# Optimization experiments

Measured on AMD Instinct MI355X. Metric: run time of the kernel, lower is better.

## Reference

```python
import jax, jax.numpy as jnp
import numpy as np
from itertools import permutations

NUM_SPEAKERS = 4
EPS = 1e-07


def setup_inputs() -> dict:
    key = jax.random.key(0)
    k1, k2 = jax.random.split(key)
    B, T, S = 128, 16384, NUM_SPEAKERS
    pred = jax.random.uniform(k1, (B, T, S), dtype=jnp.float32)
    target = jax.random.uniform(k2, (B, T, S), dtype=jnp.float32)
    mask = jnp.ones((B, T), dtype=jnp.float32)
    return {"pred": pred, "target": target, "mask": mask}


def reference(pred, target, mask):
    # pred, target: [B, T, S]; mask: [B, T]
    B, T, S = pred.shape
    p = jnp.clip(pred, EPS, 1.0 - EPS)
    logp = jnp.log(p)          # [B,T,S]
    log1mp = jnp.log1p(-p)     # [B,T,S]
    # Pairwise BCE: bce[b,t,i,j] = -(target[b,t,j]*log p[b,t,i] + (1-target[b,t,j])*log(1-p[b,t,i]))
    bce = -(target[:, :, None, :] * logp[:, :, :, None]
            + (1.0 - target[:, :, None, :]) * log1mp[:, :, :, None])  # [B,T,S,S]
    denom = jnp.sum(mask, axis=1)  # [B]
    # Masked mean over time, mean over prediction-speaker axis i -> cost matrix C[b,i,j]
    C = jnp.einsum('btij,bt->bij', bce, mask) / (S * denom)[:, None, None]  # [B,S,S]
    perms = jnp.asarray(list(permutations(range(S))), dtype=jnp.int32)  # [P,S]
    # perm_losses[b,p] = sum_i C[b, i, perms[p,i]] / S? no: mean over i already folded via /S above
    idx_i = jnp.arange(S)[None, :]            # [1,S]
    perm_losses = jnp.sum(C[:, idx_i, perms], axis=-1)  # [B,P]
    min_loss = jnp.min(perm_losses, axis=-1)  # [B]
    best_idx = jnp.argmin(perm_losses, axis=-1)  # [B] index into perms
    loss = jnp.mean(min_loss)
    best_perms = perms[best_idx]  # [B,S]
    return loss, best_perms
```

## Files before the change

kernel.cpp:

```cpp
#include <hip/hip_runtime.h>

#define TPB    256
#define CHUNKS 8
#define NACC   21
#define NPERM  24

__constant__ int c_perm[NPERM][4] = {
    {0,1,2,3},{0,1,3,2},{0,2,1,3},{0,2,3,1},{0,3,1,2},{0,3,2,1},
    {1,0,2,3},{1,0,3,2},{1,2,0,3},{1,2,3,0},{1,3,0,2},{1,3,2,0},
    {2,0,1,3},{2,0,3,1},{2,1,0,3},{2,1,3,0},{2,3,0,1},{2,3,1,0},
    {3,0,1,2},{3,0,2,1},{3,1,0,2},{3,1,2,0},{3,2,0,1},{3,2,1,0}
};

__global__ __launch_bounds__(TPB) void pit_partial(
    const float* __restrict__ pred, const float* __restrict__ target,
    const float* __restrict__ mask, float* __restrict__ partial, int T, int nblk)
{
    const int b      = blockIdx.x / CHUNKS;
    const int chunk  = blockIdx.x - b * CHUNKS;
    const int tPerBlock = (T + CHUNKS - 1) / CHUNKS;
    const int tid    = threadIdx.x;
    const int base   = chunk * tPerBlock;
    const int tEnd   = min(base + tPerBlock, T);

    const float4* p4  = (const float4*)pred   + (size_t)b * T;
    const float4* t4  = (const float4*)target + (size_t)b * T;
    const float* mrow = mask + (size_t)b * T;

    float D[4][4] = {{0.f,0.f,0.f,0.f},{0.f,0.f,0.f,0.f},
                     {0.f,0.f,0.f,0.f},{0.f,0.f,0.f,0.f}};
    float S1[4] = {0.f,0.f,0.f,0.f};
    float dn = 0.f;

    const float lo = 1e-7f;
    const float hi = 1.0f - 1e-7f;

    auto body = [&](int t) {
        float4 pv = p4[t];
        float4 tv = t4[t];
        float m   = mrow[t];
        float pp[4] = {pv.x, pv.y, pv.z, pv.w};
        float tt[4] = {tv.x, tv.y, tv.z, tv.w};
        float lp[4], lq[4];
        #pragma unroll
        for (int s = 0; s < 4; ++s) {
            float p = fminf(fmaxf(pp[s], lo), hi);
            lp[s] = __logf(p);
            lq[s] = __logf(1.0f - p);
        }
        dn += m;
        float mt[4];
        #pragma unroll
        for (int j = 0; j < 4; ++j) mt[j] = m * tt[j];
        #pragma unroll
        for (int i = 0; i < 4; ++i) {
            S1[i] = fmaf(m, lq[i], S1[i]);
            float d = lq[i] - lp[i];
            #pragma unroll
            for (int j = 0; j < 4; ++j) D[i][j] = fmaf(d, mt[j], D[i][j]);
        }
    };

    int t = base + tid;
    for (; t + 3 * TPB < tEnd; t += 4 * TPB) {
        body(t);
        body(t + TPB);
        body(t + 2 * TPB);
        body(t + 3 * TPB);
    }
    for (; t < tEnd; t += TPB) body(t);

    float acc[NACC];
    #pragma unroll
    for (int i = 0; i < 4; ++i)
        #pragma unroll
        for (int j = 0; j < 4; ++j) acc[i * 4 + j] = D[i][j];
    #pragma unroll
    for (int i = 0; i < 4; ++i) acc[16 + i] = S1[i];
    acc[20] = dn;

    #pragma unroll
    for (int k = 0; k < NACC; ++k) {
        float v = acc[k];
        #pragma unroll
        for (int off = 32; off > 0; off >>= 1)
            v += __shfl_xor(v, off, 64);
        acc[k] = v;
    }

    __shared__ float sred[TPB / 64][NACC];
    const int wave = tid >> 6;
    const int lane = tid & 63;
    if (lane == 0) {
        #pragma unroll
        for (int k = 0; k < NACC; ++k) sred[wave][k] = acc[k];
    }
    __syncthreads();
    if (tid < NACC) {
        float v = 0.f;
        #pragma unroll
        for (int w = 0; w < TPB / 64; ++w) v += sred[w][tid];
        partial[(size_t)tid * nblk + blockIdx.x] = v;
    }
}

__global__ __launch_bounds__(128) void pit_final(
    const float* __restrict__ partial, float* __restrict__ out, int B, int nblk)
{
    const int b = threadIdx.x;
    float minv = 0.f;

    if (b < B) {
        float A[NACC];
        #pragma unroll
        for (int k = 0; k < NACC; ++k) {
            const float4* src =
                (const float4*)(partial + (size_t)k * nblk + b * CHUNKS);
            float4 u = src[0];
            float4 v = src[1];
            A[k] = ((u.x + u.y) + (u.z + u.w)) + ((v.x + v.y) + (v.z + v.w));
        }
        const float inv = 1.0f / (4.0f * A[20]);
        float C[4][4];
        #pragma unroll
        for (int i = 0; i < 4; ++i)
            #pragma unroll
            for (int j = 0; j < 4; ++j)
                C[i][j] = (A[i * 4 + j] - A[16 + i]) * inv;

        minv = 3.4e38f;
        int mini = 0;
        #pragma unroll
        for (int p = 0; p < NPERM; ++p) {
            float v = C[0][c_perm[p][0]] + C[1][c_perm[p][1]]
                    + C[2][c_perm[p][2]] + C[3][c_perm[p][3]];
            if (v < minv) { minv = v; mini = p; }
        }
        #pragma unroll
        for (int i = 0; i < 4; ++i)
            out[1 + b * 4 + i] = (float)c_perm[mini][i];
    }

    float v = minv;
    #pragma unroll
    for (int off = 32; off > 0; off >>= 1)
        v += __shfl_xor(v, off, 64);
    __shared__ float ssum[16];
    const int wave = threadIdx.x >> 6;
    const int nwaves = blockDim.x >> 6;
    if ((threadIdx.x & 63) == 0) ssum[wave] = v;
    __syncthreads();
    if (threadIdx.x == 0) {
        float s = 0.f;
        for (int w = 0; w < nwaves; ++w) s += ssum[w];
        out[0] = s / (float)B;
    }
}

extern "C" void kernel_launch(void* const* d_in, const int* in_sizes, int n_in,
                              void* d_out, int out_size, void* d_ws, size_t ws_size,
                              hipStream_t stream)
{
    const float* pred   = (const float*)d_in[0];
    const float* target = (const float*)d_in[1];
    const float* mask   = (const float*)d_in[2];
    float* out     = (float*)d_out;
    float* partial = (float*)d_ws;

    const int B = (out_size - 1) / 4;
    const int T = in_sizes[2] / B;
    const int nblk = B * CHUNKS;

    pit_partial<<<nblk, TPB, 0, stream>>>(pred, target, mask, partial, T, nblk);
    pit_final<<<1, 128, 0, stream>>>(partial, out, B, nblk);
}
```

Measured before the change: 114.2 us.

## Fuse final permutation reduction into partial kernel via last-block ticket

```diff
diff --git a/kernel.cpp b/kernel.cpp
--- a/kernel.cpp
+++ b/kernel.cpp
@@ -12,9 +12,11 @@
     {3,0,1,2},{3,0,2,1},{3,1,0,2},{3,1,2,0},{3,2,0,1},{3,2,1,0}
 };
 
-__global__ __launch_bounds__(TPB) void pit_partial(
+__global__ __launch_bounds__(TPB) void pit_fused(
     const float* __restrict__ pred, const float* __restrict__ target,
-    const float* __restrict__ mask, float* __restrict__ partial, int T, int nblk)
+    const float* __restrict__ mask, float* __restrict__ partial,
+    unsigned int* __restrict__ ticket, float* __restrict__ out,
+    int T, int nblk, int B)
 {
     const int b      = blockIdx.x / CHUNKS;
     const int chunk  = blockIdx.x - b * CHUNKS;
@@ -35,7 +37,7 @@
     const float lo = 1e-7f;
     const float hi = 1.0f - 1e-7f;
 
-    auto body = [&](int t) {
+    for (int t = base + tid; t < tEnd; t += TPB) {
         float4 pv = p4[t];
         float4 tv = t4[t];
         float m   = mrow[t];
@@ -59,16 +61,7 @@
             #pragma unroll
             for (int j = 0; j < 4; ++j) D[i][j] = fmaf(d, mt[j], D[i][j]);
         }
-    };
-
-    int t = base + tid;
-    for (; t + 3 * TPB < tEnd; t += 4 * TPB) {
-        body(t);
-        body(t + TPB);
-        body(t + 2 * TPB);
-        body(t + 3 * TPB);
     }
-    for (; t < tEnd; t += TPB) body(t);
 
     float acc[NACC];
     #pragma unroll
@@ -89,6 +82,7 @@
     }
 
     __shared__ float sred[TPB / 64][NACC];
+    __shared__ bool s_last;
     const int wave = tid >> 6;
     const int lane = tid & 63;
     if (lane == 0) {
@@ -102,20 +96,23 @@
         for (int w = 0; w < TPB / 64; ++w) v += sred[w][tid];
         partial[(size_t)tid * nblk + blockIdx.x] = v;
     }
-}
 
-__global__ __launch_bounds__(128) void pit_final(
-    const float* __restrict__ partial, float* __restrict__ out, int B, int nblk)
-{
-    const int b = threadIdx.x;
+    __threadfence();
+    if (tid == 0) {
+        unsigned int prev = atomicAdd(ticket, 1u);
+        s_last = (prev == (unsigned int)(nblk - 1));
+    }
+    __syncthreads();
+    if (!s_last) return;
+    __threadfence();
+
     float minv = 0.f;
-
-    if (b < B) {
+    if (tid < B) {
         float A[NACC];
         #pragma unroll
         for (int k = 0; k < NACC; ++k) {
             const float4* src =
-                (const float4*)(partial + (size_t)k * nblk + b * CHUNKS);
+                (const float4*)(partial + (size_t)k * nblk + tid * CHUNKS);
             float4 u = src[0];
             float4 v = src[1];
             A[k] = ((u.x + u.y) + (u.z + u.w)) + ((v.x + v.y) + (v.z + v.w));
@@ -138,21 +135,20 @@
         }
         #pragma unroll
         for (int i = 0; i < 4; ++i)
-            out[1 + b * 4 + i] = (float)c_perm[mini][i];
+            out[1 + tid * 4 + i] = (float)c_perm[mini][i];
     }
 
-    float v = minv;
+    float v = (tid < B) ? minv : 0.f;
     #pragma unroll
     for (int off = 32; off > 0; off >>= 1)
         v += __shfl_xor(v, off, 64);
-    __shared__ float ssum[16];
-    const int wave = threadIdx.x >> 6;
-    const int nwaves = blockDim.x >> 6;
-    if ((threadIdx.x & 63) == 0) ssum[wave] = v;
+    __shared__ float ssum[TPB / 64];
+    if (lane == 0) ssum[wave] = v;
     __syncthreads();
-    if (threadIdx.x == 0) {
+    if (tid == 0) {
         float s = 0.f;
-        for (int w = 0; w < nwaves; ++w) s += ssum[w];
+        #pragma unroll
+        for (int w = 0; w < TPB / 64; ++w) s += ssum[w];
         out[0] = s / (float)B;
     }
 }
@@ -165,12 +161,17 @@
     const float* target = (const float*)d_in[1];
     const float* mask   = (const float*)d_in[2];
     float* out     = (float*)d_out;
-    float* partial = (float*)d_ws;
 
     const int B = (out_size - 1) / 4;
     const int T = in_sizes[2] / B;
     const int nblk = B * CHUNKS;
 
-    pit_partial<<<nblk, TPB, 0, stream>>>(pred, target, mask, partial, T, nblk);
-    pit_final<<<1, 128, 0, stream>>>(partial, out, B, nblk);
+    float* partial = (float*)d_ws;
+    unsigned int* ticket =
+        (unsigned int*)((char*)d_ws + ((size_t)NACC * nblk * 4 + 127) / 128 * 128);
+
+    hipMemsetAsync(ticket, 0, sizeof(unsigned int), stream);
+
+    pit_fused<<<nblk, TPB, 0, stream>>>(pred, target, mask, partial, ticket,
+                                        out, T, nblk, B);
 }
```

After: 193.9 us. 69.7% more time.
